# Optimization experiments

Measured on AMD Instinct MI355X. Metric: run time of the kernel, lower is better.

## Reference

```python
import jax, jax.numpy as jnp
import numpy as np

B, L, D, H = 16, 4096, 512, 512
TEMP, THRESH, PRIOR = 1.0, 0.5, 0.25


def setup_inputs() -> dict:
    key = jax.random.key(0)
    k1, k2, k3, k4, k5 = jax.random.split(key, 5)
    hidden = jax.random.normal(k1, (B, L, D), jnp.float32)
    # variable-length sequences: lengths in [L/2, L]
    lengths = jax.random.randint(k2, (B,), L // 2, L + 1)
    attention_mask = (jnp.arange(L)[None, :] < lengths[:, None]).astype(jnp.float32)
    # uniform noise for RelaxedBernoulli rsample (logistic reparameterization)
    u = jax.random.uniform(k3, (B, L), jnp.float32, 1e-6, 1.0 - 1e-6)
    w1 = jax.random.normal(k4, (D, H), jnp.float32) * (1.0 / np.sqrt(D))
    b1 = jnp.zeros((H,), jnp.float32)
    w2 = jax.random.normal(k5, (H, 1), jnp.float32) * (1.0 / np.sqrt(H))
    b2 = jnp.full((1,), 3.0, jnp.float32)  # init_for_12: bias filled with +3
    return dict(hidden=hidden, attention_mask=attention_mask, u=u,
                w1=w1, b1=b1, w2=w2, b2=b2)


def _binomial_loss(k, n, p):
    # -log Binomial(n, p).pmf(k) / n
    log_coef = (jax.lax.lgamma(n + 1.0) - jax.lax.lgamma(k + 1.0)
                - jax.lax.lgamma(n - k + 1.0))
    return -(log_coef + k * jnp.log(p) + (n - k) * jnp.log1p(-p)) / n


def _forward(hidden, attention_mask, u, w1, b1, w2, b2):
    # boundary MLP -> logits (B, L)
    logits = (jax.nn.relu(hidden @ w1 + b1) @ w2 + b2)[..., 0]
    # RelaxedBernoulli(temp, probs=sigmoid(logits)).rsample():
    # sigmoid((logits + logistic_noise) / temp)
    logistic = jnp.log(u) - jnp.log1p(-u)
    soft = jax.nn.sigmoid((logits + logistic) / TEMP) * attention_mask
    hard = (soft > THRESH).astype(hidden.dtype) * attention_mask
    # force a boundary on the last real token of each sequence
    pad = attention_mask == 0
    first_pad = pad & (jnp.cumsum(pad.astype(jnp.int32), axis=1) == 1)
    last_real = jnp.roll(first_pad, -1, axis=1).at[:, -1].set(False).astype(hidden.dtype)
    hard = jnp.maximum(hard, last_real)
    soft = jnp.maximum(soft, last_real)
    # straight-through estimator
    hard_b = hard - jax.lax.stop_gradient(soft) + soft
    masked_hidden = hidden * attention_mask[..., None]
    # segment id of token t = #boundaries strictly before t (boundary closes its segment)
    hard_sg = jax.lax.stop_gradient(hard)
    seg = (jnp.cumsum(hard_sg, axis=1) - hard_sg).astype(jnp.int32)  # (B, L)

    def pool_one(x, sid):
        # x: (L, D), sid: (L,) -> mean pool per segment, padded to L segments
        s = jax.ops.segment_sum(x, sid, num_segments=L)
        c = jax.ops.segment_sum(jnp.ones((L,), x.dtype), sid, num_segments=L)
        return s / jnp.maximum(c, 1.0)[:, None]

    pooled = jax.vmap(pool_one)(masked_hidden, seg)  # (B, L, D), first nb[b] rows valid
    nb = hard_sg.sum(axis=1)  # per-example boundary count
    valid = jnp.arange(L)[None, :] < nb[:, None]
    pooled = pooled * valid[..., None]
    shortened_attention_mask = valid.astype(attention_mask.dtype)  # padded to L
    k = hard_b.sum()
    n = attention_mask.sum()
    loss = _binomial_loss(k, n, PRIOR)
    return pooled, loss, k, n, shortened_attention_mask


def reference(hidden, attention_mask, u, w1, b1, w2, b2):
    return _forward(hidden, attention_mask, u, w1, b1, w2, b2)
```

## Files before the change

kernel.cpp:

```cpp
#include <hip/hip_runtime.h>
#include <hip/hip_bf16.h>
#include <stdint.h>

#define BB 16
#define LL 4096
#define DD 512
#define HH 512
#define MM (BB * LL)
#define NTILES_H 8

typedef _Float16 f16x8 __attribute__((ext_vector_type(8)));
typedef float f32x4 __attribute__((ext_vector_type(4)));

__global__ __launch_bounds__(256) void convb_len_kernel(
    const float* __restrict__ W1, _Float16* __restrict__ Bh, _Float16* __restrict__ Bl,
    const float* __restrict__ mask, int* __restrict__ lenb)
{
    if (blockIdx.x == 128) {
        const int b = threadIdx.x;
        if (b < BB) {
            const float* row = mask + b * LL;
            int lo = 0, hi = LL;
            while (lo < hi) {
                const int mid = (lo + hi) >> 1;
                if (row[mid] == 0.0f) hi = mid; else lo = mid + 1;
            }
            lenb[b] = lo;
        }
        return;
    }
    const int t    = blockIdx.x * 256 + threadIdx.x;
    const int tile = t >> 9;
    const int u    = t & 511;
    const int nl   = u >> 2;
    const int q    = u & 3;
    const int ht   = tile >> 4;
    const int kt   = tile & 15;
    const int g    = q ^ (nl & 3) ^ ((nl >> 2) & 3);

    const int n = ht * 128 + nl;
    const int kbase = kt * 32;
    f16x8 h, l;
#pragma unroll
    for (int e = 0; e < 8; ++e) {
        const int k = kbase + ((e < 4) ? (4 * g + e) : (16 + 4 * g + (e - 4)));
        const float v = W1[(size_t)k * HH + n] * 64.0f;
        const _Float16 hh = (_Float16)v;
        const float r = v - (float)hh;
        h[e] = hh;
        l[e] = (_Float16)(r * 4096.0f);
    }
    *reinterpret_cast<f16x8*>(Bh + (size_t)tile * 4096 + u * 8) = h;
    *reinterpret_cast<f16x8*>(Bl + (size_t)tile * 4096 + u * 8) = l;
}

__device__ __forceinline__ void gload16(const void* g, void* l)
{
    __builtin_amdgcn_global_load_lds(
        (const __attribute__((address_space(1))) unsigned int*)g,
        (__attribute__((address_space(3))) unsigned int*)l, 16, 0, 0);
}

__global__ __launch_bounds__(256, 2) void gemm_mfma_kernel(
    const float* __restrict__ A,
    const _Float16* __restrict__ Bh, const _Float16* __restrict__ Bl,
    const float* __restrict__ B1,    const float* __restrict__ W2,
    float* __restrict__ part)
{
    __shared__ __align__(16) char lds[2][32768];

    const int d  = blockIdx.x;
    const int x  = d & 7;
    const int ht = (d >> 3) & 3;
    const int mt = x * 64 + (d >> 5);

    const int tid  = threadIdx.x;
    const int lane = tid & 63;
    const int w    = tid >> 6;
    const int wr   = w >> 1;
    const int wc   = w & 1;
    const int c    = lane & 15;
    const int g    = lane >> 4;

    int aoff0[4], aoff1[4], boff[4];
    const int qb = g ^ (c & 3) ^ ((c >> 2) & 3);
#pragma unroll
    for (int f = 0; f < 4; ++f) {
        const int r = wr * 64 + f * 16 + c;
        aoff0[f] = r * 128 + ((g ^ (c & 7)) << 4);
        aoff1[f] = r * 128 + (((g + 4) ^ (c & 7)) << 4);
        const int n_local = wc * 64 + f * 16 + c;
        boff[f] = n_local * 64 + (qb << 4);
    }

    f32x4 accM[4][4] = {};
    f32x4 accL[4][4] = {};

    auto stage = [&](int kt, int bsel) {
        char* l = &lds[bsel][0];
#pragma unroll
        for (int i = 0; i < 4; ++i) {
            const int s   = tid + i * 256;
            const int row = s >> 3;
            const int kc  = (s & 7) ^ (row & 7);
            gload16(A + ((size_t)(mt * 128 + row)) * DD + kt * 32 + kc * 4,
                    l + s * 16);
        }
        const _Float16* s2 = Bh + ((size_t)(ht * 16 + kt)) * 4096;
        const _Float16* s3 = Bl + ((size_t)(ht * 16 + kt)) * 4096;
#pragma unroll
        for (int i = 0; i < 2; ++i) {
            const int s = tid + i * 256;
            gload16(s2 + s * 8, l + 16384 + s * 16);
            gload16(s3 + s * 8, l + 24576 + s * 16);
        }
    };

    stage(0, 0);
    int buf = 0;
    for (int kt = 0; kt < 16; ++kt) {
        __syncthreads();
        if (kt + 1 < 16) stage(kt + 1, buf ^ 1);
        const char* base = &lds[buf][0];

        f16x8 ah[4], al[4];
#pragma unroll
        for (int mf = 0; mf < 4; ++mf) {
            const f32x4 v0 = *reinterpret_cast<const f32x4*>(base + aoff0[mf]);
            const f32x4 v1 = *reinterpret_cast<const f32x4*>(base + aoff1[mf]);
            const float v[8] = {v0[0], v0[1], v0[2], v0[3], v1[0], v1[1], v1[2], v1[3]};
            f16x8 h, lo;
#pragma unroll
            for (int e = 0; e < 8; ++e) {
                const _Float16 hh = (_Float16)v[e];
                h[e]  = hh;
                lo[e] = (_Float16)((v[e] - (float)hh) * 4096.0f);
            }
            ah[mf] = h;
            al[mf] = lo;
        }
#pragma unroll
        for (int nf = 0; nf < 4; ++nf) {
            const f16x8 bh = *reinterpret_cast<const f16x8*>(base + 16384 + boff[nf]);
            const f16x8 bl = *reinterpret_cast<const f16x8*>(base + 24576 + boff[nf]);
#pragma unroll
            for (int mf = 0; mf < 4; ++mf) {
                accM[mf][nf] = __builtin_amdgcn_mfma_f32_16x16x32_f16(ah[mf], bh, accM[mf][nf], 0, 0, 0);
                accL[mf][nf] = __builtin_amdgcn_mfma_f32_16x16x32_f16(ah[mf], bl, accL[mf][nf], 0, 0, 0);
                accL[mf][nf] = __builtin_amdgcn_mfma_f32_16x16x32_f16(al[mf], bh, accL[mf][nf], 0, 0, 0);
            }
        }
        buf ^= 1;
    }

    float w2v[4], b1v[4];
#pragma unroll
    for (int nf = 0; nf < 4; ++nf) {
        const int n = ht * 128 + wc * 64 + nf * 16 + c;
        w2v[nf] = W2[n];
        b1v[nf] = B1[n];
    }
    float red[4][4];
#pragma unroll
    for (int mf = 0; mf < 4; ++mf)
#pragma unroll
        for (int r = 0; r < 4; ++r) {
            float s = 0.0f;
#pragma unroll
            for (int nf = 0; nf < 4; ++nf) {
                float y = (accM[mf][nf][r] + accL[mf][nf][r] * (1.0f / 4096.0f)) * (1.0f / 64.0f) + b1v[nf];
                y = (y > 0.0f) ? y : 0.0f;
                s = fmaf(y, w2v[nf], s);
            }
            red[mf][r] = s;
        }
#pragma unroll
    for (int step = 1; step < 16; step <<= 1)
#pragma unroll
        for (int mf = 0; mf < 4; ++mf)
#pragma unroll
            for (int r = 0; r < 4; ++r)
                red[mf][r] += __shfl_xor(red[mf][r], step);
    if (c == 0) {
        const int p = ht * 2 + wc;
#pragma unroll
        for (int mf = 0; mf < 4; ++mf)
#pragma unroll
            for (int r = 0; r < 4; ++r) {
                const int m = mt * 128 + wr * 64 + mf * 16 + g * 4 + r;
                part[(size_t)p * MM + m] = red[mf][r];
            }
    }
}

#define BM 64
#define BN 64
#define BK 32

__global__ __launch_bounds__(256) void mlp_gemm_kernel(
    const float* __restrict__ A, const float* __restrict__ W1,
    const float* __restrict__ B1, const float* __restrict__ W2,
    float* __restrict__ part)
{
    __shared__ __align__(16) float As[BK][BM];
    __shared__ __align__(16) float Bs[BK][BN];
    __shared__ float red[64][17];

    const int ht = blockIdx.x;
    const int mt = blockIdx.y;
    const int t  = threadIdx.x;
    const int tx = t & 15;
    const int ty = t >> 4;
    const int row0 = mt * BM;
    const int n0   = ht * BN;

    float acc[4][4];
#pragma unroll
    for (int i = 0; i < 4; ++i)
#pragma unroll
        for (int j = 0; j < 4; ++j) acc[i][j] = 0.0f;

    for (int k0 = 0; k0 < DD; k0 += BK) {
#pragma unroll
        for (int i = 0; i < 2; ++i) {
            const int idx = t + i * 256;
            const int m   = idx >> 3;
            const int kq  = idx & 7;
            const float4 a = *reinterpret_cast<const float4*>(
                &A[(size_t)(row0 + m) * DD + k0 + kq * 4]);
            As[kq * 4 + 0][m] = a.x;
            As[kq * 4 + 1][m] = a.y;
            As[kq * 4 + 2][m] = a.z;
            As[kq * 4 + 3][m] = a.w;
        }
#pragma unroll
        for (int i = 0; i < 2; ++i) {
            const int idx = t + i * 256;
            const int kk  = idx >> 4;
            const int nq  = idx & 15;
            const float4 bv = *reinterpret_cast<const float4*>(
                &W1[(size_t)(k0 + kk) * HH + n0 + nq * 4]);
            *reinterpret_cast<float4*>(&Bs[kk][nq * 4]) = bv;
        }
        __syncthreads();
#pragma unroll
        for (int k = 0; k < BK; ++k) {
            const float4 av = *reinterpret_cast<const float4*>(&As[k][ty * 4]);
            const float4 bv = *reinterpret_cast<const float4*>(&Bs[k][tx * 4]);
            const float a[4]  = {av.x, av.y, av.z, av.w};
            const float bb[4] = {bv.x, bv.y, bv.z, bv.w};
#pragma unroll
            for (int i = 0; i < 4; ++i)
#pragma unroll
                for (int j = 0; j < 4; ++j)
                    acc[i][j] = fmaf(a[i], bb[j], acc[i][j]);
        }
        __syncthreads();
    }

    const float4 b1v = *reinterpret_cast<const float4*>(&B1[n0 + tx * 4]);
    const float4 w2v = *reinterpret_cast<const float4*>(&W2[n0 + tx * 4]);
    const float b1a[4] = {b1v.x, b1v.y, b1v.z, b1v.w};
    const float w2a[4] = {w2v.x, w2v.y, w2v.z, w2v.w};
#pragma unroll
    for (int i = 0; i < 4; ++i) {
        float p = 0.0f;
#pragma unroll
        for (int j = 0; j < 4; ++j) {
            float y = acc[i][j] + b1a[j];
            y = (y > 0.0f) ? y : 0.0f;
            p = fmaf(y, w2a[j], p);
        }
        red[ty * 4 + i][tx] = p;
    }
    __syncthreads();
    if (t < 64) {
        float s = 0.0f;
#pragma unroll
        for (int q = 0; q < 16; ++q) s += red[t][q];
        part[(size_t)ht * MM + row0 + t] = s;
    }
}

__global__ __launch_bounds__(1024) void rowscan_kernel(
    const float* __restrict__ part, const float* __restrict__ u,
    const float* __restrict__ b2,   const int* __restrict__ lenb,
    int* __restrict__ bpos, int* __restrict__ nb, float* __restrict__ smask_out)
{
    __shared__ int wtot[16];
    const int b    = blockIdx.x;
    const int tid  = threadIdx.x;
    const int lane = tid & 63;
    const int wid  = tid >> 6;
    const int base = b * LL;
    const int len  = lenb[b];
    const float b2v = b2[0];

    int h[4];
    int cnt = 0;
#pragma unroll
    for (int j = 0; j < 4; ++j) {
        const int l = tid * 4 + j;
        float logit = b2v;
#pragma unroll
        for (int p = 0; p < NTILES_H; ++p) logit += part[(size_t)p * MM + base + l];
        const float uu = u[base + l];
        const float xx = logit + logf(uu) - log1pf(-uu);
        int hh = (xx > 0.0f && l < len) ? 1 : 0;
        if (len < LL && l == len - 1) hh = 1;
        h[j] = hh;
        cnt += hh;
    }

    int incl = cnt;
#pragma unroll
    for (int s = 1; s < 64; s <<= 1) {
        const int v = __shfl_up(incl, s);
        if (lane >= s) incl += v;
    }
    if (lane == 63) wtot[wid] = incl;
    __syncthreads();

    int woff = 0, tot = 0;
#pragma unroll
    for (int i = 0; i < 16; ++i) {
        const int wi = wtot[i];
        woff += (i < wid) ? wi : 0;
        tot  += wi;
    }

    int pos = woff + incl - cnt;
#pragma unroll
    for (int j = 0; j < 4; ++j) {
        if (h[j]) {
            bpos[base + pos] = tid * 4 + j;
            ++pos;
        }
    }
#pragma unroll
    for (int j = 0; j < 4; ++j) {
        const int l = tid * 4 + j;
        smask_out[base + l] = (l < tot) ? 1.0f : 0.0f;
    }
    if (tid == 0) nb[b] = tot;
}

__global__ __launch_bounds__(128) void pool_kernel(
    const float* __restrict__ hidden, const int* __restrict__ bpos,
    const int* __restrict__ nb, float* __restrict__ out)
{
    const int blk = blockIdx.x;
    const int b   = blk >> 12;
    const int s   = blk & (LL - 1);
    const int tid = threadIdx.x;
    const int base = b * LL;

    float ax = 0.0f, ay = 0.0f, az = 0.0f, aw = 0.0f;
    const int n = nb[b];
    if (s < n) {
        const int start = (s == 0) ? 0 : (bpos[base + s - 1] + 1);
        const int end   = bpos[base + s];
        const float inv = 1.0f / (float)(end - start + 1);
        for (int tkn = start; tkn <= end; ++tkn) {
            const float4 v = *reinterpret_cast<const float4*>(
                &hidden[((size_t)(base + tkn)) * DD + tid * 4]);
            ax += v.x; ay += v.y; az += v.z; aw += v.w;
        }
        ax *= inv; ay *= inv; az *= inv; aw *= inv;
    }
    float4 r; r.x = ax; r.y = ay; r.z = az; r.w = aw;
    *reinterpret_cast<float4*>(&out[((size_t)(base + s)) * DD + tid * 4]) = r;
}

__global__ void finalize_kernel(
    const int* __restrict__ nb, const int* __restrict__ lenb,
    float* __restrict__ out)
{
    if (threadIdx.x == 0 && blockIdx.x == 0) {
        int k = 0, n = 0;
        for (int b = 0; b < BB; ++b) { k += nb[b]; n += lenb[b]; }
        const double dk = (double)k, dn = (double)n, p = 0.25;
        const double logc = lgamma(dn + 1.0) - lgamma(dk + 1.0) - lgamma(dn - dk + 1.0);
        const double loss = -(logc + dk * log(p) + (dn - dk) * log1p(-p)) / dn;
        out[0] = (float)loss;
        out[1] = (float)k;
        out[2] = (float)n;
    }
}

extern "C" void kernel_launch(void* const* d_in, const int* in_sizes, int n_in,
                              void* d_out, int out_size, void* d_ws, size_t ws_size,
                              hipStream_t stream) {
    const float* hidden = (const float*)d_in[0];
    const float* mask   = (const float*)d_in[1];
    const float* u      = (const float*)d_in[2];
    const float* w1     = (const float*)d_in[3];
    const float* b1     = (const float*)d_in[4];
    const float* w2     = (const float*)d_in[5];
    const float* b2     = (const float*)d_in[6];
    float* out = (float*)d_out;

    const size_t BH_BYTES   = (size_t)64 * 4096 * 2;
    const size_t PART_BYTES = (size_t)NTILES_H * MM * 4;
    const size_t BPOS_BYTES = (size_t)MM * 4;
    const size_t need = BH_BYTES * 2 + PART_BYTES + BPOS_BYTES + 4096;

    const size_t P = (size_t)MM * DD;
    float* smask = out + P + 3;

    char* ws = (char*)d_ws;
    const bool fast = (ws_size >= need);

    char* tail = fast ? (ws + BH_BYTES * 2) : ws;
    float* part = (float*)tail;
    int*   bpos = (int*)(tail + PART_BYTES);
    int*   nbuf = (int*)(tail + PART_BYTES + BPOS_BYTES);
    int*   lenb = nbuf + BB;

    if (fast) {
        _Float16* Bh = (_Float16*)ws;
        _Float16* Bl = (_Float16*)(ws + BH_BYTES);
        convb_len_kernel<<<129, 256, 0, stream>>>(w1, Bh, Bl, mask, lenb);
        gemm_mfma_kernel<<<2048, 256, 0, stream>>>(hidden, Bh, Bl, b1, w2, part);
    } else {
        convb_len_kernel<<<129, 256, 0, stream>>>(w1, (_Float16*)ws, (_Float16*)ws, mask, lenb);
        mlp_gemm_kernel<<<dim3(NTILES_H, MM / BM), 256, 0, stream>>>(hidden, w1, b1, w2, part);
    }

    rowscan_kernel<<<BB, 1024, 0, stream>>>(part, u, b2, lenb, bpos, nbuf, smask);
    pool_kernel<<<MM, 128, 0, stream>>>(hidden, bpos, nbuf, out);
    finalize_kernel<<<1, 64, 0, stream>>>(nbuf, lenb, out + P);
}
```

Baseline: 332.3 us.

## Give each GEMM wave full N width and batch pooling segments per block

The MFMA GEMM warp layout changes from a 2x2 split (64 rows x 64 cols per wave) to 4x1 (32 rows x 128 cols per wave). Each wave now reduces all 128 hidden columns of its tile itself, which halves the partial-sum buffers that rowscan must add (np=4). The pool kernel now has each wave handle 8 segments with 2 float4 loads per lane, instead of one 128-thread block per segment, and the finalize kernel is folded into it to save a launch. The trade-offs are that each wave converts fewer A rows per B fragment load, and the pool blocks may end up unevenly loaded.

After: 339.7 us. 1.02x slower.

```diff
diff --git a/kernel.cpp b/kernel.cpp
--- a/kernel.cpp
+++ b/kernel.cpp
@@ -7,7 +7,6 @@
 #define DD 512
 #define HH 512
 #define MM (BB * LL)
-#define NTILES_H 8
 
 typedef _Float16 f16x8 __attribute__((ext_vector_type(8)));
 typedef float f32x4 __attribute__((ext_vector_type(4)));
@@ -77,24 +76,23 @@
     const int tid  = threadIdx.x;
     const int lane = tid & 63;
     const int w    = tid >> 6;
-    const int wr   = w >> 1;
-    const int wc   = w & 1;
     const int c    = lane & 15;
     const int g    = lane >> 4;
 
-    int aoff0[4], aoff1[4], boff[4];
+    int aoff[2][2], boff[8];
     const int qb = g ^ (c & 3) ^ ((c >> 2) & 3);
 #pragma unroll
-    for (int f = 0; f < 4; ++f) {
-        const int r = wr * 64 + f * 16 + c;
-        aoff0[f] = r * 128 + ((g ^ (c & 7)) << 4);
-        aoff1[f] = r * 128 + (((g + 4) ^ (c & 7)) << 4);
-        const int n_local = wc * 64 + f * 16 + c;
-        boff[f] = n_local * 64 + (qb << 4);
-    }
-
-    f32x4 accM[4][4] = {};
-    f32x4 accL[4][4] = {};
+    for (int mf = 0; mf < 2; ++mf) {
+        const int r = w * 32 + mf * 16 + c;
+        aoff[mf][0] = r * 128 + ((g ^ (c & 7)) << 4);
+        aoff[mf][1] = r * 128 + (((g + 4) ^ (c & 7)) << 4);
+    }
+#pragma unroll
+    for (int nf = 0; nf < 8; ++nf)
+        boff[nf] = (nf * 16 + c) * 64 + (qb << 4);
+
+    f32x4 accM[2][8] = {};
+    f32x4 accL[2][8] = {};
 
     auto stage = [&](int kt, int bsel) {
         char* l = &lds[bsel][0];
@@ -123,11 +121,11 @@
         if (kt + 1 < 16) stage(kt + 1, buf ^ 1);
         const char* base = &lds[buf][0];
 
-        f16x8 ah[4], al[4];
-#pragma unroll
-        for (int mf = 0; mf < 4; ++mf) {
-            const f32x4 v0 = *reinterpret_cast<const f32x4*>(base + aoff0[mf]);
-            const f32x4 v1 = *reinterpret_cast<const f32x4*>(base + aoff1[mf]);
+        f16x8 ah[2], al[2];
+#pragma unroll
+        for (int mf = 0; mf < 2; ++mf) {
+            const f32x4 v0 = *reinterpret_cast<const f32x4*>(base + aoff[mf][0]);
+            const f32x4 v1 = *reinterpret_cast<const f32x4*>(base + aoff[mf][1]);
             const float v[8] = {v0[0], v0[1], v0[2], v0[3], v1[0], v1[1], v1[2], v1[3]};
             f16x8 h, lo;
 #pragma unroll
@@ -140,11 +138,11 @@
             al[mf] = lo;
         }
 #pragma unroll
-        for (int nf = 0; nf < 4; ++nf) {
+        for (int nf = 0; nf < 8; ++nf) {
             const f16x8 bh = *reinterpret_cast<const f16x8*>(base + 16384 + boff[nf]);
             const f16x8 bl = *reinterpret_cast<const f16x8*>(base + 24576 + boff[nf]);
 #pragma unroll
-            for (int mf = 0; mf < 4; ++mf) {
+            for (int mf = 0; mf < 2; ++mf) {
                 accM[mf][nf] = __builtin_amdgcn_mfma_f32_16x16x32_f16(ah[mf], bh, accM[mf][nf], 0, 0, 0);
                 accL[mf][nf] = __builtin_amdgcn_mfma_f32_16x16x32_f16(ah[mf], bl, accL[mf][nf], 0, 0, 0);
                 accL[mf][nf] = __builtin_amdgcn_mfma_f32_16x16x32_f16(al[mf], bh, accL[mf][nf], 0, 0, 0);
@@ -153,21 +151,21 @@
         buf ^= 1;
     }
 
-    float w2v[4], b1v[4];
-#pragma unroll
-    for (int nf = 0; nf < 4; ++nf) {
-        const int n = ht * 128 + wc * 64 + nf * 16 + c;
+    float w2v[8], b1v[8];
+#pragma unroll
+    for (int nf = 0; nf < 8; ++nf) {
+        const int n = ht * 128 + nf * 16 + c;
         w2v[nf] = W2[n];
         b1v[nf] = B1[n];
     }
-    float red[4][4];
-#pragma unroll
-    for (int mf = 0; mf < 4; ++mf)
+    float red[2][4];
+#pragma unroll
+    for (int mf = 0; mf < 2; ++mf)
 #pragma unroll
         for (int r = 0; r < 4; ++r) {
             float s = 0.0f;
 #pragma unroll
-            for (int nf = 0; nf < 4; ++nf) {
+            for (int nf = 0; nf < 8; ++nf) {
                 float y = (accM[mf][nf][r] + accL[mf][nf][r] * (1.0f / 4096.0f)) * (1.0f / 64.0f) + b1v[nf];
                 y = (y > 0.0f) ? y : 0.0f;
                 s = fmaf(y, w2v[nf], s);
@@ -177,18 +175,17 @@
 #pragma unroll
     for (int step = 1; step < 16; step <<= 1)
 #pragma unroll
-        for (int mf = 0; mf < 4; ++mf)
+        for (int mf = 0; mf < 2; ++mf)
 #pragma unroll
             for (int r = 0; r < 4; ++r)
                 red[mf][r] += __shfl_xor(red[mf][r], step);
     if (c == 0) {
-        const int p = ht * 2 + wc;
-#pragma unroll
-        for (int mf = 0; mf < 4; ++mf)
+#pragma unroll
+        for (int mf = 0; mf < 2; ++mf)
 #pragma unroll
             for (int r = 0; r < 4; ++r) {
-                const int m = mt * 128 + wr * 64 + mf * 16 + g * 4 + r;
-                part[(size_t)p * MM + m] = red[mf][r];
+                const int m = mt * 128 + w * 32 + mf * 16 + g * 4 + r;
+                part[(size_t)ht * MM + m] = red[mf][r];
             }
     }
 }
@@ -285,7 +282,8 @@
 __global__ __launch_bounds__(1024) void rowscan_kernel(
     const float* __restrict__ part, const float* __restrict__ u,
     const float* __restrict__ b2,   const int* __restrict__ lenb,
-    int* __restrict__ bpos, int* __restrict__ nb, float* __restrict__ smask_out)
+    int* __restrict__ bpos, int* __restrict__ nb, float* __restrict__ smask_out,
+    int np)
 {
     __shared__ int wtot[16];
     const int b    = blockIdx.x;
@@ -302,8 +300,7 @@
     for (int j = 0; j < 4; ++j) {
         const int l = tid * 4 + j;
         float logit = b2v;
-#pragma unroll
-        for (int p = 0; p < NTILES_H; ++p) logit += part[(size_t)p * MM + base + l];
+        for (int p = 0; p < np; ++p) logit += part[(size_t)p * MM + base + l];
         const float uu = u[base + l];
         const float xx = logit + logf(uu) - log1pf(-uu);
         int hh = (xx > 0.0f && l < len) ? 1 : 0;
@@ -345,46 +342,50 @@
     if (tid == 0) nb[b] = tot;
 }
 
-__global__ __launch_bounds__(128) void pool_kernel(
+__global__ __launch_bounds__(256) void pool_kernel(
     const float* __restrict__ hidden, const int* __restrict__ bpos,
-    const int* __restrict__ nb, float* __restrict__ out)
-{
-    const int blk = blockIdx.x;
-    const int b   = blk >> 12;
-    const int s   = blk & (LL - 1);
-    const int tid = threadIdx.x;
+    const int* __restrict__ nb, const int* __restrict__ lenb,
+    float* __restrict__ out, float* __restrict__ scal)
+{
+    const int blk  = blockIdx.x;
+    const int b    = blk >> 7;
+    const int s0   = (blk & 127) * 32;
+    const int w    = threadIdx.x >> 6;
+    const int lane = threadIdx.x & 63;
     const int base = b * LL;
-
-    float ax = 0.0f, ay = 0.0f, az = 0.0f, aw = 0.0f;
-    const int n = nb[b];
-    if (s < n) {
-        const int start = (s == 0) ? 0 : (bpos[base + s - 1] + 1);
-        const int end   = bpos[base + s];
-        const float inv = 1.0f / (float)(end - start + 1);
-        for (int tkn = start; tkn <= end; ++tkn) {
-            const float4 v = *reinterpret_cast<const float4*>(
-                &hidden[((size_t)(base + tkn)) * DD + tid * 4]);
-            ax += v.x; ay += v.y; az += v.z; aw += v.w;
-        }
-        ax *= inv; ay *= inv; az *= inv; aw *= inv;
-    }
-    float4 r; r.x = ax; r.y = ay; r.z = az; r.w = aw;
-    *reinterpret_cast<float4*>(&out[((size_t)(base + s)) * DD + tid * 4]) = r;
-}
-
-__global__ void finalize_kernel(
-    const int* __restrict__ nb, const int* __restrict__ lenb,
-    float* __restrict__ out)
-{
-    if (threadIdx.x == 0 && blockIdx.x == 0) {
-        int k = 0, n = 0;
-        for (int b = 0; b < BB; ++b) { k += nb[b]; n += lenb[b]; }
-        const double dk = (double)k, dn = (double)n, p = 0.25;
+    const int n    = nb[b];
+
+    if (blk == 0 && threadIdx.x == 0) {
+        int k = 0, nn = 0;
+        for (int i = 0; i < BB; ++i) { k += nb[i]; nn += lenb[i]; }
+        const double dk = (double)k, dn = (double)nn, p = 0.25;
         const double logc = lgamma(dn + 1.0) - lgamma(dk + 1.0) - lgamma(dn - dk + 1.0);
         const double loss = -(logc + dk * log(p) + (dn - dk) * log1p(-p)) / dn;
-        out[0] = (float)loss;
-        out[1] = (float)k;
-        out[2] = (float)n;
+        scal[0] = (float)loss;
+        scal[1] = (float)k;
+        scal[2] = (float)nn;
+    }
+
+    for (int i = 0; i < 8; ++i) {
+        const int s = s0 + w * 8 + i;
+        f32x4 a0 = {0.0f, 0.0f, 0.0f, 0.0f};
+        f32x4 a1 = {0.0f, 0.0f, 0.0f, 0.0f};
+        if (s < n) {
+            const int start = (s == 0) ? 0 : (bpos[base + s - 1] + 1);
+            const int end   = bpos[base + s];
+            for (int tkn = start; tkn <= end; ++tkn) {
+                const f32x4* row = reinterpret_cast<const f32x4*>(
+                    &hidden[((size_t)(base + tkn)) * DD]);
+                a0 += row[lane];
+                a1 += row[lane + 64];
+            }
+            const float inv = 1.0f / (float)(end - start + 1);
+            a0 *= inv;
+            a1 *= inv;
+        }
+        f32x4* orow = reinterpret_cast<f32x4*>(&out[((size_t)(base + s)) * DD]);
+        orow[lane]      = a0;
+        orow[lane + 64] = a1;
     }
 }
 
@@ -401,7 +402,7 @@
     float* out = (float*)d_out;
 
     const size_t BH_BYTES   = (size_t)64 * 4096 * 2;
-    const size_t PART_BYTES = (size_t)NTILES_H * MM * 4;
+    const size_t PART_BYTES = (size_t)8 * MM * 4;
     const size_t BPOS_BYTES = (size_t)MM * 4;
     const size_t need = BH_BYTES * 2 + PART_BYTES + BPOS_BYTES + 4096;
 
@@ -417,17 +418,19 @@
     int*   nbuf = (int*)(tail + PART_BYTES + BPOS_BYTES);
     int*   lenb = nbuf + BB;
 
+    int np;
     if (fast) {
         _Float16* Bh = (_Float16*)ws;
         _Float16* Bl = (_Float16*)(ws + BH_BYTES);
         convb_len_kernel<<<129, 256, 0, stream>>>(w1, Bh, Bl, mask, lenb);
         gemm_mfma_kernel<<<2048, 256, 0, stream>>>(hidden, Bh, Bl, b1, w2, part);
+        np = 4;
     } else {
         convb_len_kernel<<<129, 256, 0, stream>>>(w1, (_Float16*)ws, (_Float16*)ws, mask, lenb);
-        mlp_gemm_kernel<<<dim3(NTILES_H, MM / BM), 256, 0, stream>>>(hidden, w1, b1, w2, part);
-    }
-
-    rowscan_kernel<<<BB, 1024, 0, stream>>>(part, u, b2, lenb, bpos, nbuf, smask);
-    pool_kernel<<<MM, 128, 0, stream>>>(hidden, bpos, nbuf, out);
-    finalize_kernel<<<1, 64, 0, stream>>>(nbuf, lenb, out + P);
-}
+        mlp_gemm_kernel<<<dim3(8, MM / BM), 256, 0, stream>>>(hidden, w1, b1, w2, part);
+        np = 8;
+    }
+
+    rowscan_kernel<<<BB, 1024, 0, stream>>>(part, u, b2, lenb, bpos, nbuf, smask, np);
+    pool_kernel<<<2048, 256, 0, stream>>>(hidden, bpos, nbuf, lenb, out, out + P);
+}
```

## Load GEMM operands directly from global into registers, dropping LDS staging

Applied to the files above, without the earlier changes.

The MFMA GEMM no longer double-buffers A and the fp16 hi/lo W1 tiles through LDS. Each wave now loads its own 32 rows of A and all 128 columns of B straight from global memory into registers. The wave tiling changes from 2x2 (64x64 per wave) to 4x1 (32x128 per wave), so partial sums fall from 8 to 4 per row and rowscan is templated on the partial count. This removes LDS traffic, barriers and swizzle arithmetic, at the cost of redundant global/L2 reads of B across waves and uncoalesced strided A loads with no prefetch overlap.

Result: slower. 410.5 us (+23.5%).

```diff
diff --git a/kernel.cpp b/kernel.cpp
--- a/kernel.cpp
+++ b/kernel.cpp
@@ -7,7 +7,6 @@
 #define DD 512
 #define HH 512
 #define MM (BB * LL)
-#define NTILES_H 8
 
 typedef _Float16 f16x8 __attribute__((ext_vector_type(8)));
 typedef float f32x4 __attribute__((ext_vector_type(4)));
@@ -36,14 +35,13 @@
     const int q    = u & 3;
     const int ht   = tile >> 4;
     const int kt   = tile & 15;
-    const int g    = q ^ (nl & 3) ^ ((nl >> 2) & 3);
 
     const int n = ht * 128 + nl;
     const int kbase = kt * 32;
     f16x8 h, l;
 #pragma unroll
     for (int e = 0; e < 8; ++e) {
-        const int k = kbase + ((e < 4) ? (4 * g + e) : (16 + 4 * g + (e - 4)));
+        const int k = kbase + ((e < 4) ? (4 * q + e) : (16 + 4 * q + (e - 4)));
         const float v = W1[(size_t)k * HH + n] * 64.0f;
         const _Float16 hh = (_Float16)v;
         const float r = v - (float)hh;
@@ -54,120 +52,85 @@
     *reinterpret_cast<f16x8*>(Bl + (size_t)tile * 4096 + u * 8) = l;
 }
 
-__device__ __forceinline__ void gload16(const void* g, void* l)
-{
-    __builtin_amdgcn_global_load_lds(
-        (const __attribute__((address_space(1))) unsigned int*)g,
-        (__attribute__((address_space(3))) unsigned int*)l, 16, 0, 0);
-}
-
 __global__ __launch_bounds__(256, 2) void gemm_mfma_kernel(
     const float* __restrict__ A,
     const _Float16* __restrict__ Bh, const _Float16* __restrict__ Bl,
     const float* __restrict__ B1,    const float* __restrict__ W2,
     float* __restrict__ part)
 {
-    __shared__ __align__(16) char lds[2][32768];
-
     const int d  = blockIdx.x;
     const int x  = d & 7;
     const int ht = (d >> 3) & 3;
     const int mt = x * 64 + (d >> 5);
 
-    const int tid  = threadIdx.x;
-    const int lane = tid & 63;
-    const int w    = tid >> 6;
-    const int wr   = w >> 1;
-    const int wc   = w & 1;
+    const int lane = threadIdx.x & 63;
+    const int w    = threadIdx.x >> 6;
     const int c    = lane & 15;
     const int g    = lane >> 4;
 
-    int aoff0[4], aoff1[4], boff[4];
-    const int qb = g ^ (c & 3) ^ ((c >> 2) & 3);
-#pragma unroll
-    for (int f = 0; f < 4; ++f) {
-        const int r = wr * 64 + f * 16 + c;
-        aoff0[f] = r * 128 + ((g ^ (c & 7)) << 4);
-        aoff1[f] = r * 128 + (((g + 4) ^ (c & 7)) << 4);
-        const int n_local = wc * 64 + f * 16 + c;
-        boff[f] = n_local * 64 + (qb << 4);
-    }
-
-    f32x4 accM[4][4] = {};
-    f32x4 accL[4][4] = {};
-
-    auto stage = [&](int kt, int bsel) {
-        char* l = &lds[bsel][0];
-#pragma unroll
-        for (int i = 0; i < 4; ++i) {
-            const int s   = tid + i * 256;
-            const int row = s >> 3;
-            const int kc  = (s & 7) ^ (row & 7);
-            gload16(A + ((size_t)(mt * 128 + row)) * DD + kt * 32 + kc * 4,
-                    l + s * 16);
-        }
-        const _Float16* s2 = Bh + ((size_t)(ht * 16 + kt)) * 4096;
-        const _Float16* s3 = Bl + ((size_t)(ht * 16 + kt)) * 4096;
-#pragma unroll
-        for (int i = 0; i < 2; ++i) {
-            const int s = tid + i * 256;
-            gload16(s2 + s * 8, l + 16384 + s * 16);
-            gload16(s3 + s * 8, l + 24576 + s * 16);
-        }
-    };
-
-    stage(0, 0);
-    int buf = 0;
+    const float* arow0 = A + ((size_t)(mt * 128 + w * 32 + c)) * DD;
+    const float* arow1 = arow0 + (size_t)16 * DD;
+    const _Float16* bhb = Bh + ((size_t)(ht * 16)) * 4096 + ((size_t)(c * 4 + g)) * 8;
+    const _Float16* blb = Bl + ((size_t)(ht * 16)) * 4096 + ((size_t)(c * 4 + g)) * 8;
+
+    f32x4 accM[2][8] = {};
+    f32x4 accL[2][8] = {};
+
     for (int kt = 0; kt < 16; ++kt) {
-        __syncthreads();
-        if (kt + 1 < 16) stage(kt + 1, buf ^ 1);
-        const char* base = &lds[buf][0];
-
-        f16x8 ah[4], al[4];
-#pragma unroll
-        for (int mf = 0; mf < 4; ++mf) {
-            const f32x4 v0 = *reinterpret_cast<const f32x4*>(base + aoff0[mf]);
-            const f32x4 v1 = *reinterpret_cast<const f32x4*>(base + aoff1[mf]);
-            const float v[8] = {v0[0], v0[1], v0[2], v0[3], v1[0], v1[1], v1[2], v1[3]};
-            f16x8 h, lo;
-#pragma unroll
-            for (int e = 0; e < 8; ++e) {
-                const _Float16 hh = (_Float16)v[e];
-                h[e]  = hh;
-                lo[e] = (_Float16)((v[e] - (float)hh) * 4096.0f);
-            }
-            ah[mf] = h;
-            al[mf] = lo;
-        }
-#pragma unroll
-        for (int nf = 0; nf < 4; ++nf) {
-            const f16x8 bh = *reinterpret_cast<const f16x8*>(base + 16384 + boff[nf]);
-            const f16x8 bl = *reinterpret_cast<const f16x8*>(base + 24576 + boff[nf]);
-#pragma unroll
-            for (int mf = 0; mf < 4; ++mf) {
+        const f32x4 a00 = *reinterpret_cast<const f32x4*>(arow0 + kt * 32 + 4 * g);
+        const f32x4 a01 = *reinterpret_cast<const f32x4*>(arow0 + kt * 32 + 16 + 4 * g);
+        const f32x4 a10 = *reinterpret_cast<const f32x4*>(arow1 + kt * 32 + 4 * g);
+        const f32x4 a11 = *reinterpret_cast<const f32x4*>(arow1 + kt * 32 + 16 + 4 * g);
+
+        f16x8 ah[2], al[2];
+        {
+            const float v[2][8] = {
+                {a00[0], a00[1], a00[2], a00[3], a01[0], a01[1], a01[2], a01[3]},
+                {a10[0], a10[1], a10[2], a10[3], a11[0], a11[1], a11[2], a11[3]}};
+#pragma unroll
+            for (int mf = 0; mf < 2; ++mf) {
+                f16x8 h, lo;
+#pragma unroll
+                for (int e = 0; e < 8; ++e) {
+                    const _Float16 hh = (_Float16)v[mf][e];
+                    h[e]  = hh;
+                    lo[e] = (_Float16)((v[mf][e] - (float)hh) * 4096.0f);
+                }
+                ah[mf] = h;
+                al[mf] = lo;
+            }
+        }
+
+        const _Float16* bhk = bhb + (size_t)kt * 4096;
+        const _Float16* blk = blb + (size_t)kt * 4096;
+#pragma unroll
+        for (int nf = 0; nf < 8; ++nf) {
+            const f16x8 bh = *reinterpret_cast<const f16x8*>(bhk + nf * 512);
+            const f16x8 bl = *reinterpret_cast<const f16x8*>(blk + nf * 512);
+#pragma unroll
+            for (int mf = 0; mf < 2; ++mf) {
                 accM[mf][nf] = __builtin_amdgcn_mfma_f32_16x16x32_f16(ah[mf], bh, accM[mf][nf], 0, 0, 0);
                 accL[mf][nf] = __builtin_amdgcn_mfma_f32_16x16x32_f16(ah[mf], bl, accL[mf][nf], 0, 0, 0);
                 accL[mf][nf] = __builtin_amdgcn_mfma_f32_16x16x32_f16(al[mf], bh, accL[mf][nf], 0, 0, 0);
             }
         }
-        buf ^= 1;
-    }
-
-    float w2v[4], b1v[4];
-#pragma unroll
-    for (int nf = 0; nf < 4; ++nf) {
-        const int n = ht * 128 + wc * 64 + nf * 16 + c;
+    }
+
+    float w2v[8], b1v[8];
+#pragma unroll
+    for (int nf = 0; nf < 8; ++nf) {
+        const int n = ht * 128 + nf * 16 + c;
         w2v[nf] = W2[n];
         b1v[nf] = B1[n];
     }
-    float red[4][4];
-#pragma unroll
-    for (int mf = 0; mf < 4; ++mf)
+    float red[2][4];
+#pragma unroll
+    for (int mf = 0; mf < 2; ++mf)
 #pragma unroll
         for (int r = 0; r < 4; ++r) {
             float s = 0.0f;
 #pragma unroll
-            for (int nf = 0; nf < 4; ++nf) {
+            for (int nf = 0; nf < 8; ++nf) {
                 float y = (accM[mf][nf][r] + accL[mf][nf][r] * (1.0f / 4096.0f)) * (1.0f / 64.0f) + b1v[nf];
                 y = (y > 0.0f) ? y : 0.0f;
                 s = fmaf(y, w2v[nf], s);
@@ -177,18 +140,17 @@
 #pragma unroll
     for (int step = 1; step < 16; step <<= 1)
 #pragma unroll
-        for (int mf = 0; mf < 4; ++mf)
+        for (int mf = 0; mf < 2; ++mf)
 #pragma unroll
             for (int r = 0; r < 4; ++r)
                 red[mf][r] += __shfl_xor(red[mf][r], step);
     if (c == 0) {
-        const int p = ht * 2 + wc;
-#pragma unroll
-        for (int mf = 0; mf < 4; ++mf)
+#pragma unroll
+        for (int mf = 0; mf < 2; ++mf)
 #pragma unroll
             for (int r = 0; r < 4; ++r) {
-                const int m = mt * 128 + wr * 64 + mf * 16 + g * 4 + r;
-                part[(size_t)p * MM + m] = red[mf][r];
+                const int m = mt * 128 + w * 32 + mf * 16 + g * 4 + r;
+                part[(size_t)ht * MM + m] = red[mf][r];
             }
     }
 }
@@ -282,6 +244,7 @@
     }
 }
 
+template <int NP>
 __global__ __launch_bounds__(1024) void rowscan_kernel(
     const float* __restrict__ part, const float* __restrict__ u,
     const float* __restrict__ b2,   const int* __restrict__ lenb,
@@ -303,7 +266,7 @@
         const int l = tid * 4 + j;
         float logit = b2v;
 #pragma unroll
-        for (int p = 0; p < NTILES_H; ++p) logit += part[(size_t)p * MM + base + l];
+        for (int p = 0; p < NP; ++p) logit += part[(size_t)p * MM + base + l];
         const float uu = u[base + l];
         const float xx = logit + logf(uu) - log1pf(-uu);
         int hh = (xx > 0.0f && l < len) ? 1 : 0;
@@ -401,7 +364,7 @@
     float* out = (float*)d_out;
 
     const size_t BH_BYTES   = (size_t)64 * 4096 * 2;
-    const size_t PART_BYTES = (size_t)NTILES_H * MM * 4;
+    const size_t PART_BYTES = (size_t)8 * MM * 4;
     const size_t BPOS_BYTES = (size_t)MM * 4;
     const size_t need = BH_BYTES * 2 + PART_BYTES + BPOS_BYTES + 4096;
 
@@ -422,12 +385,13 @@
         _Float16* Bl = (_Float16*)(ws + BH_BYTES);
         convb_len_kernel<<<129, 256, 0, stream>>>(w1, Bh, Bl, mask, lenb);
         gemm_mfma_kernel<<<2048, 256, 0, stream>>>(hidden, Bh, Bl, b1, w2, part);
+        rowscan_kernel<4><<<BB, 1024, 0, stream>>>(part, u, b2, lenb, bpos, nbuf, smask);
     } else {
         convb_len_kernel<<<129, 256, 0, stream>>>(w1, (_Float16*)ws, (_Float16*)ws, mask, lenb);
-        mlp_gemm_kernel<<<dim3(NTILES_H, MM / BM), 256, 0, stream>>>(hidden, w1, b1, w2, part);
-    }
-
-    rowscan_kernel<<<BB, 1024, 0, stream>>>(part, u, b2, lenb, bpos, nbuf, smask);
+        mlp_gemm_kernel<<<dim3(8, MM / BM), 256, 0, stream>>>(hidden, w1, b1, w2, part);
+        rowscan_kernel<8><<<BB, 1024, 0, stream>>>(part, u, b2, lenb, bpos, nbuf, smask);
+    }
+
     pool_kernel<<<MM, 128, 0, stream>>>(hidden, bpos, nbuf, out);
     finalize_kernel<<<1, 64, 0, stream>>>(nbuf, lenb, out + P);
 }
```

## Load GEMM A operand directly from global into registers, stage only B in LDS

Applied to the files above, without the earlier changes.

The MFMA GEMM kernel now reads the fp32 hidden-state A fragments straight from global memory into registers each k-step instead of staging them through LDS with swizzled async copies. This halves the LDS footprint per block and removes A-side LDS traffic, and the barrier is moved after the A loads. The risk is that the global loads are now exposed latency inside the loop without double buffering, and each lane fetches only 16-byte chunks per row, so coalescing is poorer. The rowscan kernel is templated on the partial count, with no functional change.

Result: slower. 383.3 us (+15.3%).

```diff
diff --git a/kernel.cpp b/kernel.cpp
--- a/kernel.cpp
+++ b/kernel.cpp
@@ -7,7 +7,6 @@
 #define DD 512
 #define HH 512
 #define MM (BB * LL)
-#define NTILES_H 8
 
 typedef _Float16 f16x8 __attribute__((ext_vector_type(8)));
 typedef float f32x4 __attribute__((ext_vector_type(4)));
@@ -67,7 +66,7 @@
     const float* __restrict__ B1,    const float* __restrict__ W2,
     float* __restrict__ part)
 {
-    __shared__ __align__(16) char lds[2][32768];
+    __shared__ __align__(16) char lds[2][16384];
 
     const int d  = blockIdx.x;
     const int x  = d & 7;
@@ -82,53 +81,41 @@
     const int c    = lane & 15;
     const int g    = lane >> 4;
 
-    int aoff0[4], aoff1[4], boff[4];
+    int boff[4];
     const int qb = g ^ (c & 3) ^ ((c >> 2) & 3);
 #pragma unroll
-    for (int f = 0; f < 4; ++f) {
-        const int r = wr * 64 + f * 16 + c;
-        aoff0[f] = r * 128 + ((g ^ (c & 7)) << 4);
-        aoff1[f] = r * 128 + (((g + 4) ^ (c & 7)) << 4);
-        const int n_local = wc * 64 + f * 16 + c;
-        boff[f] = n_local * 64 + (qb << 4);
-    }
+    for (int nf = 0; nf < 4; ++nf)
+        boff[nf] = (wc * 64 + nf * 16 + c) * 64 + (qb << 4);
+
+    const float* arow[4];
+#pragma unroll
+    for (int mf = 0; mf < 4; ++mf)
+        arow[mf] = A + ((size_t)(mt * 128 + wr * 64 + mf * 16 + c)) * DD;
 
     f32x4 accM[4][4] = {};
     f32x4 accL[4][4] = {};
 
-    auto stage = [&](int kt, int bsel) {
+    auto stageB = [&](int kt, int bsel) {
         char* l = &lds[bsel][0];
-#pragma unroll
-        for (int i = 0; i < 4; ++i) {
-            const int s   = tid + i * 256;
-            const int row = s >> 3;
-            const int kc  = (s & 7) ^ (row & 7);
-            gload16(A + ((size_t)(mt * 128 + row)) * DD + kt * 32 + kc * 4,
-                    l + s * 16);
-        }
         const _Float16* s2 = Bh + ((size_t)(ht * 16 + kt)) * 4096;
         const _Float16* s3 = Bl + ((size_t)(ht * 16 + kt)) * 4096;
 #pragma unroll
         for (int i = 0; i < 2; ++i) {
             const int s = tid + i * 256;
-            gload16(s2 + s * 8, l + 16384 + s * 16);
-            gload16(s3 + s * 8, l + 24576 + s * 16);
+            gload16(s2 + s * 8, l + s * 16);
+            gload16(s3 + s * 8, l + 8192 + s * 16);
         }
     };
 
-    stage(0, 0);
+    stageB(0, 0);
     int buf = 0;
     for (int kt = 0; kt < 16; ++kt) {
-        __syncthreads();
-        if (kt + 1 < 16) stage(kt + 1, buf ^ 1);
-        const char* base = &lds[buf][0];
-
         f16x8 ah[4], al[4];
 #pragma unroll
         for (int mf = 0; mf < 4; ++mf) {
-            const f32x4 v0 = *reinterpret_cast<const f32x4*>(base + aoff0[mf]);
-            const f32x4 v1 = *reinterpret_cast<const f32x4*>(base + aoff1[mf]);
-            const float v[8] = {v0[0], v0[1], v0[2], v0[3], v1[0], v1[1], v1[2], v1[3]};
+            const f32x4 a0 = *reinterpret_cast<const f32x4*>(arow[mf] + kt * 32 + 4 * g);
+            const f32x4 a1 = *reinterpret_cast<const f32x4*>(arow[mf] + kt * 32 + 16 + 4 * g);
+            const float v[8] = {a0[0], a0[1], a0[2], a0[3], a1[0], a1[1], a1[2], a1[3]};
             f16x8 h, lo;
 #pragma unroll
             for (int e = 0; e < 8; ++e) {
@@ -139,10 +126,15 @@
             ah[mf] = h;
             al[mf] = lo;
         }
+
+        __syncthreads();
+        if (kt + 1 < 16) stageB(kt + 1, buf ^ 1);
+        const char* base = &lds[buf][0];
+
 #pragma unroll
         for (int nf = 0; nf < 4; ++nf) {
-            const f16x8 bh = *reinterpret_cast<const f16x8*>(base + 16384 + boff[nf]);
-            const f16x8 bl = *reinterpret_cast<const f16x8*>(base + 24576 + boff[nf]);
+            const f16x8 bh = *reinterpret_cast<const f16x8*>(base + boff[nf]);
+            const f16x8 bl = *reinterpret_cast<const f16x8*>(base + 8192 + boff[nf]);
 #pragma unroll
             for (int mf = 0; mf < 4; ++mf) {
                 accM[mf][nf] = __builtin_amdgcn_mfma_f32_16x16x32_f16(ah[mf], bh, accM[mf][nf], 0, 0, 0);
@@ -282,6 +274,7 @@
     }
 }
 
+template <int NP>
 __global__ __launch_bounds__(1024) void rowscan_kernel(
     const float* __restrict__ part, const float* __restrict__ u,
     const float* __restrict__ b2,   const int* __restrict__ lenb,
@@ -303,7 +296,7 @@
         const int l = tid * 4 + j;
         float logit = b2v;
 #pragma unroll
-        for (int p = 0; p < NTILES_H; ++p) logit += part[(size_t)p * MM + base + l];
+        for (int p = 0; p < NP; ++p) logit += part[(size_t)p * MM + base + l];
         const float uu = u[base + l];
         const float xx = logit + logf(uu) - log1pf(-uu);
         int hh = (xx > 0.0f && l < len) ? 1 : 0;
@@ -401,7 +394,7 @@
     float* out = (float*)d_out;
 
     const size_t BH_BYTES   = (size_t)64 * 4096 * 2;
-    const size_t PART_BYTES = (size_t)NTILES_H * MM * 4;
+    const size_t PART_BYTES = (size_t)8 * MM * 4;
     const size_t BPOS_BYTES = (size_t)MM * 4;
     const size_t need = BH_BYTES * 2 + PART_BYTES + BPOS_BYTES + 4096;
 
@@ -422,12 +415,13 @@
         _Float16* Bl = (_Float16*)(ws + BH_BYTES);
         convb_len_kernel<<<129, 256, 0, stream>>>(w1, Bh, Bl, mask, lenb);
         gemm_mfma_kernel<<<2048, 256, 0, stream>>>(hidden, Bh, Bl, b1, w2, part);
+        rowscan_kernel<8><<<BB, 1024, 0, stream>>>(part, u, b2, lenb, bpos, nbuf, smask);
     } else {
         convb_len_kernel<<<129, 256, 0, stream>>>(w1, (_Float16*)ws, (_Float16*)ws, mask, lenb);
-        mlp_gemm_kernel<<<dim3(NTILES_H, MM / BM), 256, 0, stream>>>(hidden, w1, b1, w2, part);
-    }
-
-    rowscan_kernel<<<BB, 1024, 0, stream>>>(part, u, b2, lenb, bpos, nbuf, smask);
+        mlp_gemm_kernel<<<dim3(8, MM / BM), 256, 0, stream>>>(hidden, w1, b1, w2, part);
+        rowscan_kernel<8><<<BB, 1024, 0, stream>>>(part, u, b2, lenb, bpos, nbuf, smask);
+    }
+
     pool_kernel<<<MM, 128, 0, stream>>>(hidden, bpos, nbuf, out);
     finalize_kernel<<<1, 64, 0, stream>>>(nbuf, lenb, out + P);
 }
```
